# Kernel optimization log

Hardware: AMD Instinct MI355X
Metric: run time of the kernel (lower is better)

## Reference

```python
import jax, jax.numpy as jnp
import numpy as np

# Model dims (match init_kwargs / input_specs)
T, N, E, F_IN, F_OUT, BW = 16, 50000, 131072, 64, 64, 3


def setup_inputs() -> dict:
    key = jax.random.key(0)
    ks = jax.random.split(key, 6)
    x = jax.random.normal(ks[0], (T, N, F_IN), dtype=jnp.float32)
    M = jax.random.normal(ks[1], (T, T), dtype=jnp.float32)
    adj_rows = jax.random.randint(ks[2], (T, E), 0, N, dtype=jnp.int32)
    adj_cols = jax.random.randint(ks[3], (T, E), 0, N, dtype=jnp.int32)
    adj_vals = jax.random.uniform(ks[4], (T, E), dtype=jnp.float32)
    lim = float(np.sqrt(6.0 / (F_IN + F_OUT)))  # xavier_uniform
    weight = jax.random.uniform(ks[5], (F_IN, F_OUT), minval=-lim, maxval=lim, dtype=jnp.float32)
    return {"x": x, "M": M, "adj_vals": adj_vals, "weight": weight,
            "adj_rows": adj_rows, "adj_cols": adj_cols}


def _spmm(vals, rows, cols, x):
    # COO sparse [N,N] @ dense [N,F]: gather source rows, scatter-add to dest rows.
    return jax.ops.segment_sum(vals[:, None] * x[cols], rows, num_segments=x.shape[0])


def reference(x, M, adj_vals, weight, adj_rows, adj_cols):
    Tn, Nn, F = x.shape
    # Xt = M @ X (full M, as in compute_AtXt)
    Xt = (M @ x.reshape(Tn, -1)).reshape(Tn, Nn, F)
    k_idx = jnp.arange(Tn)
    AtXt = jnp.zeros((Tn, Nn, F), dtype=x.dtype)
    # Banded combination: At[k] = sum_{d=0}^{BW-1, k-d>=0} M[k, k-d] * A[k-d]
    # so At[k] @ Xt[k] = sum_d M[k,k-d] * (A[k-d] @ Xt[k])  -- avoids materializing At.
    for d in range(BW):
        j = k_idx - d
        valid = j >= 0
        jc = jnp.maximum(j, 0)
        w = jnp.where(valid, M[k_idx, jc], 0.0)  # [T] banded weights
        contrib = jax.vmap(_spmm)(adj_vals[jc], adj_rows[jc], adj_cols[jc], Xt)  # [T,N,F]
        AtXt = AtXt + w[:, None, None] * contrib
    # dropout is identity in eval mode; final dense projection
    return AtXt @ weight  # [T, N, F_OUT]
```

## Files before the change

kernel.cpp:

```cpp
#include <hip/hip_runtime.h>

#define TT 16
#define NN 50000
#define FF 64
#define EE 131072
#define NEDGE (TT*EE)
#define RPB 32
#define NRANGE ((NN + RPB - 1) / RPB)
#define NSUB 8
#define BCAP 256
#define NBUCK (NRANGE*NSUB)
#define SLOTS (NSUB*BCAP)
#define EMAX 1791
#define TAILI (EMAX*2)
#define K1BLKS 6250
#define APPBLKS (NEDGE/256)

typedef __attribute__((ext_vector_type(8))) short bf16x8;
typedef __attribute__((ext_vector_type(4))) short bf16x4;
typedef __attribute__((ext_vector_type(4))) float f32x4;
typedef __attribute__((ext_vector_type(2))) int   i32x2;
typedef __attribute__((ext_vector_type(2))) unsigned u32x2;

__device__ __forceinline__ unsigned pack2bf(float a, float b) {
    unsigned ua = __float_as_uint(a) + 0x8000u;
    unsigned ub = __float_as_uint(b) + 0x8000u;
    return __builtin_amdgcn_perm(ub, ua, 0x07060302u);
}
__device__ __forceinline__ float lo16f(unsigned u) { return __uint_as_float(u << 16); }
__device__ __forceinline__ float hi16f(unsigned u) { return __uint_as_float(u & 0xFFFF0000u); }

union U8 { unsigned u[4]; bf16x8 v; };
union U4 { unsigned u[2]; bf16x4 v; };

__device__ __forceinline__ f32x4 mfma16x16x16bf16(bf16x4 a, bf16x4 b, f32x4 c) {
#if __has_builtin(__builtin_amdgcn_mfma_f32_16x16x16bf16_1k)
    return __builtin_amdgcn_mfma_f32_16x16x16bf16_1k(a, b, c, 0, 0, 0);
#elif __has_builtin(__builtin_amdgcn_mfma_f32_16x16x16_bf16)
    return __builtin_amdgcn_mfma_f32_16x16x16_bf16(a, b, c, 0, 0, 0);
#else
    f32x4 d;
    asm volatile("v_mfma_f32_16x16x16_bf16 %0, %1, %2, %3\n\ts_nop 7\n\ts_nop 7"
                 : "=&v"(d) : "v"(a), "v"(b), "v"(c));
    return d;
#endif
}

__global__ __launch_bounds__(256) void k1_append(
    const float* __restrict__ x, const float* __restrict__ M,
    const float* __restrict__ W, unsigned short* __restrict__ Yt,
    const int* __restrict__ rows, const int* __restrict__ cols,
    const float* __restrict__ vals, int* __restrict__ bcnt,
    i32x2* __restrict__ btmp)
{
    if (blockIdx.x < K1BLKS) {
        const int tid  = threadIdx.x;
        const int wid  = tid >> 6;
        const int lane = tid & 63;
        const int col  = lane & 15;
        const int grp  = lane >> 4;

        bf16x8 bw[2][4];
#pragma unroll
        for (int q = 0; q < 2; ++q)
#pragma unroll
            for (int t = 0; t < 4; ++t) {
                U8 w8;
#pragma unroll
                for (int p = 0; p < 4; ++p)
                    w8.u[p] = pack2bf(W[(q*32 + grp*8 + 2*p)*FF + t*16 + col],
                                      W[(q*32 + grp*8 + 2*p + 1)*FF + t*16 + col]);
                bw[q][t] = w8.v;
            }

        U4 m4;
        m4.u[0] = pack2bf(M[col*16 + grp*4 + 0], M[col*16 + grp*4 + 1]);
        m4.u[1] = pack2bf(M[col*16 + grp*4 + 2], M[col*16 + grp*4 + 3]);
        const bf16x4 mf = m4.v;

        const f32x4 zero = {0.f, 0.f, 0.f, 0.f};
        const int node = (blockIdx.x*4 + wid)*2;
        const size_t lane_off = (size_t)col*NN*FF + grp*8;

        const float* xa = x + lane_off + (size_t)node*FF;
        f32x4 va0 = __builtin_nontemporal_load(reinterpret_cast<const f32x4*>(xa));
        f32x4 va1 = __builtin_nontemporal_load(reinterpret_cast<const f32x4*>(xa + 4));
        f32x4 va2 = __builtin_nontemporal_load(reinterpret_cast<const f32x4*>(xa + 32));
        f32x4 va3 = __builtin_nontemporal_load(reinterpret_cast<const f32x4*>(xa + 36));
        f32x4 vb0 = __builtin_nontemporal_load(reinterpret_cast<const f32x4*>(xa + 64));
        f32x4 vb1 = __builtin_nontemporal_load(reinterpret_cast<const f32x4*>(xa + 68));
        f32x4 vb2 = __builtin_nontemporal_load(reinterpret_cast<const f32x4*>(xa + 96));
        f32x4 vb3 = __builtin_nontemporal_load(reinterpret_cast<const f32x4*>(xa + 100));

#pragma unroll
        for (int n2 = 0; n2 < 2; ++n2) {
            U8 a0, a1;
            if (n2 == 0) {
                a0.u[0] = pack2bf(va0[0], va0[1]); a0.u[1] = pack2bf(va0[2], va0[3]);
                a0.u[2] = pack2bf(va1[0], va1[1]); a0.u[3] = pack2bf(va1[2], va1[3]);
                a1.u[0] = pack2bf(va2[0], va2[1]); a1.u[1] = pack2bf(va2[2], va2[3]);
                a1.u[2] = pack2bf(va3[0], va3[1]); a1.u[3] = pack2bf(va3[2], va3[3]);
            } else {
                a0.u[0] = pack2bf(vb0[0], vb0[1]); a0.u[1] = pack2bf(vb0[2], vb0[3]);
                a0.u[2] = pack2bf(vb1[0], vb1[1]); a0.u[3] = pack2bf(vb1[2], vb1[3]);
                a1.u[0] = pack2bf(vb2[0], vb2[1]); a1.u[1] = pack2bf(vb2[2], vb2[3]);
                a1.u[2] = pack2bf(vb3[0], vb3[1]); a1.u[3] = pack2bf(vb3[2], vb3[3]);
            }
            f32x4 acc[4];
#pragma unroll
            for (int t = 0; t < 4; ++t) acc[t] = zero;
#pragma unroll
            for (int t = 0; t < 4; ++t)
                acc[t] = __builtin_amdgcn_mfma_f32_16x16x32_bf16(a0.v, bw[0][t], acc[t], 0, 0, 0);
#pragma unroll
            for (int t = 0; t < 4; ++t)
                acc[t] = __builtin_amdgcn_mfma_f32_16x16x32_bf16(a1.v, bw[1][t], acc[t], 0, 0, 0);
#pragma unroll
            for (int t = 0; t < 4; ++t) {
                U4 pb;
                pb.u[0] = pack2bf(acc[t][0], acc[t][1]);
                pb.u[1] = pack2bf(acc[t][2], acc[t][3]);
                f32x4 y = mfma16x16x16bf16(pb.v, mf, zero);
                u32x2 st;
                st[0] = pack2bf(y[0], y[1]);
                st[1] = pack2bf(y[2], y[3]);
                *reinterpret_cast<u32x2*>(Yt + (size_t)(node + n2)*1024 + col*64 + t*16 + grp*4) = st;
            }
        }
    } else {
        const int i = (blockIdx.x - K1BLKS)*256 + threadIdx.x;
        const int r = __builtin_nontemporal_load(rows + i);
        const int j = i >> 17;
        const int b = (r >> 5)*NSUB + (blockIdx.x & 7);
        const int pos = atomicAdd(&bcnt[b], 1);
        if (pos < BCAP) {
            i32x2 e;
            e[0] = __builtin_nontemporal_load(cols + i) | (((r & 31)*16 + j) << 16);
            e[1] = __float_as_int(__builtin_nontemporal_load(vals + i));
            btmp[(size_t)b*BCAP + pos] = e;
        }
    }
}

__global__ __launch_bounds__(256) void sort_kernel(
    const int* __restrict__ bcnt, i32x2* __restrict__ btmp)
{
    __shared__ i32x2 sbuf[SLOTS];
    __shared__ int scnt[512], soff[512], scur[512], pscan[256];

    const int tid = threadIdx.x;
    const int blk = blockIdx.x;
    i32x2* region = btmp + (size_t)blk*SLOTS;

    scnt[tid] = 0; scnt[tid + 256] = 0;
    __syncthreads();

    int bc[NSUB]; i32x2 ent[NSUB];
#pragma unroll
    for (int s = 0; s < NSUB; ++s) {
        int c = bcnt[blk*NSUB + s];
        bc[s] = c < BCAP ? c : BCAP;
    }
#pragma unroll
    for (int s = 0; s < NSUB; ++s)
        if (tid < bc[s]) {
            ent[s] = region[s*BCAP + tid];
            atomicAdd(&scnt[((unsigned)ent[s][0]) >> 16], 1);
        }
    __syncthreads();

    const int a0 = scnt[2*tid], a1 = scnt[2*tid + 1];
    const int ps = a0 + a1;
    pscan[tid] = ps;
    __syncthreads();
    for (int o = 1; o < 256; o <<= 1) {
        int v = (tid >= o) ? pscan[tid - o] : 0;
        __syncthreads();
        pscan[tid] += v;
        __syncthreads();
    }
    const int excl = pscan[tid] - ps;
    soff[2*tid] = excl;      soff[2*tid + 1] = excl + a0;
    scur[2*tid] = excl;      scur[2*tid + 1] = excl + a0;
    __syncthreads();

#pragma unroll
    for (int s = 0; s < NSUB; ++s)
        if (tid < bc[s]) {
            const int key = ((unsigned)ent[s][0]) >> 16;
            const int pos = atomicAdd(&scur[key], 1);
            i32x2 se; se[0] = ent[s][0] & 0xFFFF; se[1] = ent[s][1];
            sbuf[pos] = se;
        }
    __syncthreads();

    const int total = soff[511] + scnt[511];
    const int lim = total < EMAX ? total : EMAX;
    for (int i = tid; i < lim; i += 256) region[i] = sbuf[i];
    int* tail = (int*)region + TAILI;
    tail[tid] = soff[tid];
    tail[tid + 256] = soff[tid + 256];
    if (tid == 0) tail[512] = lim;
}

template<int J>
__device__ __forceinline__ void k2_batch(int p0, int nj, int sbase, int esub, int fq,
    const i32x2* eb, const unsigned short* __restrict__ Yt,
    const float* __restrict__ M, f32x4* acc)
{
    const int p = p0 + esub;
    const bool act = p < nj;
    const int li = act ? (sbase + p) : 0;
    const i32x2 ent = eb[li];
    const float v = act ? __int_as_float(ent[1]) : 0.f;
    const int node = act ? ent[0] : 0;
    const unsigned short* yb = Yt + (size_t)node*1024 + J*64 + fq*4;
    {
        const u32x2 uv = *reinterpret_cast<const u32x2*>(yb);
        const float wv = M[J*17] * v;
        acc[J][0] = fmaf(wv, lo16f(uv[0]), acc[J][0]);
        acc[J][1] = fmaf(wv, hi16f(uv[0]), acc[J][1]);
        acc[J][2] = fmaf(wv, lo16f(uv[1]), acc[J][2]);
        acc[J][3] = fmaf(wv, hi16f(uv[1]), acc[J][3]);
    }
    if constexpr (J < 15) {
        const u32x2 uv = *reinterpret_cast<const u32x2*>(yb + 64);
        const float wv = M[J*17 + 16] * v;
        acc[J+1][0] = fmaf(wv, lo16f(uv[0]), acc[J+1][0]);
        acc[J+1][1] = fmaf(wv, hi16f(uv[0]), acc[J+1][1]);
        acc[J+1][2] = fmaf(wv, lo16f(uv[1]), acc[J+1][2]);
        acc[J+1][3] = fmaf(wv, hi16f(uv[1]), acc[J+1][3]);
    }
    if constexpr (J < 14) {
        const u32x2 uv = *reinterpret_cast<const u32x2*>(yb + 128);
        const float wv = M[J*17 + 32] * v;
        acc[J+2][0] = fmaf(wv, lo16f(uv[0]), acc[J+2][0]);
        acc[J+2][1] = fmaf(wv, hi16f(uv[0]), acc[J+2][1]);
        acc[J+2][2] = fmaf(wv, lo16f(uv[1]), acc[J+2][2]);
        acc[J+2][3] = fmaf(wv, hi16f(uv[1]), acc[J+2][3]);
    }
}

__global__ __launch_bounds__(256) void k2_gather(
    const unsigned short* __restrict__ Yt, const float* __restrict__ M,
    const i32x2* __restrict__ btmp, float* __restrict__ out)
{
    __shared__ i32x2 ebuf[4][128];
    const int tid  = threadIdx.x;
    const int wid  = tid >> 6;
    const int lane = tid & 63;
    const int esub = lane >> 4;
    const int fq   = lane & 15;
    const int r   = blockIdx.x*4 + wid;
    const int blk = r >> 5;
    const int rl  = r & 31;

    const i32x2* region = btmp + (size_t)blk*SLOTS;
    const int* tail = (const int*)region + TAILI;
    int o_l = 0;
    if (lane < 17) o_l = tail[rl*16 + lane];
    int off[17];
#pragma unroll
    for (int j = 0; j < 17; ++j) off[j] = __builtin_amdgcn_readlane(o_l, j);
    int ntot = off[16] - off[0];
    ntot = ntot < 128 ? ntot : 128;
    const i32x2* rowsrc = region + off[0];

    i32x2* eb = ebuf[wid];
    if (lane < ntot)      eb[lane]      = rowsrc[lane];
    if (lane + 64 < ntot) eb[lane + 64] = rowsrc[lane + 64];

    int c[16], sb[16];
#pragma unroll
    for (int j = 0; j < 16; ++j) {
        c[j]  = off[j+1] - off[j];
        sb[j] = off[j] - off[0];
    }

    f32x4 acc[16];
#pragma unroll
    for (int k = 0; k < 16; ++k) acc[k] = (f32x4){0.f, 0.f, 0.f, 0.f};

#define P1(J) k2_batch<J>(0, c[J], sb[J], esub, fq, eb, Yt, M, acc);
    P1(0)  P1(1)  P1(2)  P1(3)  P1(4)  P1(5)  P1(6)  P1(7)
    P1(8)  P1(9)  P1(10) P1(11) P1(12) P1(13) P1(14) P1(15)
#undef P1
#define P2(J) for (int p0 = 4; p0 < c[J]; p0 += 4) \
        k2_batch<J>(p0, c[J], sb[J], esub, fq, eb, Yt, M, acc);
    P2(0)  P2(1)  P2(2)  P2(3)  P2(4)  P2(5)  P2(6)  P2(7)
    P2(8)  P2(9)  P2(10) P2(11) P2(12) P2(13) P2(14) P2(15)
#undef P2

#pragma unroll
    for (int k = 0; k < 16; ++k) {
#pragma unroll
        for (int u = 0; u < 4; ++u) {
            acc[k][u] += __shfl_xor(acc[k][u], 16);
            acc[k][u] += __shfl_xor(acc[k][u], 32);
        }
    }
    if (esub == 0) {
#pragma unroll
        for (int k = 0; k < 16; ++k) {
            *reinterpret_cast<f32x4*>(out + ((size_t)k*NN + r)*FF + fq*4) = acc[k];
        }
    }
}

extern "C" void kernel_launch(void* const* d_in, const int* in_sizes, int n_in,
                              void* d_out, int out_size, void* d_ws, size_t ws_size,
                              hipStream_t stream) {
    (void)in_sizes; (void)n_in; (void)out_size; (void)ws_size;
    const float* x     = (const float*)d_in[0];
    const float* M     = (const float*)d_in[1];
    const float* avals = (const float*)d_in[2];
    const float* W     = (const float*)d_in[3];
    const int*   arows = (const int*)d_in[4];
    const int*   acols = (const int*)d_in[5];
    float* out = (float*)d_out;

    char* ws = (char*)d_ws;
    size_t o = 0;
    unsigned short* Yt = (unsigned short*)(ws + o); o += (size_t)TT*NN*FF*2;
    o = (o + 255) & ~(size_t)255;
    int* bcnt = (int*)(ws + o); o += (size_t)NBUCK*4;  o = (o + 255) & ~(size_t)255;
    i32x2* btmp = (i32x2*)(ws + o);

    (void)hipMemsetAsync(bcnt, 0, (size_t)NBUCK*4, stream);
    hipLaunchKernelGGL(k1_append, dim3(K1BLKS + APPBLKS), dim3(256), 0, stream,
                       x, M, W, Yt, arows, acols, avals, bcnt, btmp);
    hipLaunchKernelGGL(sort_kernel, dim3(NRANGE), dim3(256), 0, stream, bcnt, btmp);
    hipLaunchKernelGGL(k2_gather, dim3(12500), dim3(256), 0, stream, Yt, M, btmp, out);
}
```

Baseline: 349.8 us.

## Split fused projection/append kernel into persistent projection and separate append kernels

Splits the combined kernel into two launches: a projection-plus-time-mix kernel and a separate edge-append kernel. The projection kernel becomes grid-stride over nodes with 2048 blocks, handling one node per wave iteration instead of two nodes per wave with all loads issued up front. Nontemporal loads are replaced with ordinary loads. This adds an extra launch and removes the overlap between the memory-bound projection and the atomic-heavy append, which may expose more serialized time.

```diff
diff --git a/kernel.cpp b/kernel.cpp
--- a/kernel.cpp
+++ b/kernel.cpp
@@ -13,7 +13,6 @@
 #define SLOTS (NSUB*BCAP)
 #define EMAX 1791
 #define TAILI (EMAX*2)
-#define K1BLKS 6250
 #define APPBLKS (NEDGE/256)
 
 typedef __attribute__((ext_vector_type(8))) short bf16x8;
@@ -46,99 +45,88 @@
 #endif
 }
 
-__global__ __launch_bounds__(256) void k1_append(
+__global__ __launch_bounds__(256) void k1_proj_mix(
     const float* __restrict__ x, const float* __restrict__ M,
-    const float* __restrict__ W, unsigned short* __restrict__ Yt,
+    const float* __restrict__ W, unsigned short* __restrict__ Yt)
+{
+    const int tid  = threadIdx.x;
+    const int wid  = tid >> 6;
+    const int lane = tid & 63;
+    const int col  = lane & 15;
+    const int grp  = lane >> 4;
+
+    bf16x8 bw[2][4];
+#pragma unroll
+    for (int q = 0; q < 2; ++q)
+#pragma unroll
+        for (int t = 0; t < 4; ++t) {
+            U8 w8;
+#pragma unroll
+            for (int p = 0; p < 4; ++p)
+                w8.u[p] = pack2bf(W[(q*32 + grp*8 + 2*p)*FF + t*16 + col],
+                                  W[(q*32 + grp*8 + 2*p + 1)*FF + t*16 + col]);
+            bw[q][t] = w8.v;
+        }
+
+    U4 m4;
+    m4.u[0] = pack2bf(M[col*16 + grp*4 + 0], M[col*16 + grp*4 + 1]);
+    m4.u[1] = pack2bf(M[col*16 + grp*4 + 2], M[col*16 + grp*4 + 3]);
+    const bf16x4 mf = m4.v;
+
+    const f32x4 zero = {0.f, 0.f, 0.f, 0.f};
+    const int nwaves = gridDim.x * 4;
+
+    for (int node = blockIdx.x*4 + wid; node < NN; node += nwaves) {
+        const float* xb = x + (size_t)col*NN*FF + (size_t)node*FF + grp*8;
+        float4 v0 = *reinterpret_cast<const float4*>(xb);
+        float4 v1 = *reinterpret_cast<const float4*>(xb + 4);
+        float4 v2 = *reinterpret_cast<const float4*>(xb + 32);
+        float4 v3 = *reinterpret_cast<const float4*>(xb + 36);
+        U8 a0, a1;
+        a0.u[0] = pack2bf(v0.x, v0.y); a0.u[1] = pack2bf(v0.z, v0.w);
+        a0.u[2] = pack2bf(v1.x, v1.y); a0.u[3] = pack2bf(v1.z, v1.w);
+        a1.u[0] = pack2bf(v2.x, v2.y); a1.u[1] = pack2bf(v2.z, v2.w);
+        a1.u[2] = pack2bf(v3.x, v3.y); a1.u[3] = pack2bf(v3.z, v3.w);
+
+        f32x4 acc[4];
+#pragma unroll
+        for (int t = 0; t < 4; ++t) acc[t] = zero;
+#pragma unroll
+        for (int t = 0; t < 4; ++t)
+            acc[t] = __builtin_amdgcn_mfma_f32_16x16x32_bf16(a0.v, bw[0][t], acc[t], 0, 0, 0);
+#pragma unroll
+        for (int t = 0; t < 4; ++t)
+            acc[t] = __builtin_amdgcn_mfma_f32_16x16x32_bf16(a1.v, bw[1][t], acc[t], 0, 0, 0);
+
+#pragma unroll
+        for (int t = 0; t < 4; ++t) {
+            U4 pb;
+            pb.u[0] = pack2bf(acc[t][0], acc[t][1]);
+            pb.u[1] = pack2bf(acc[t][2], acc[t][3]);
+            f32x4 y = mfma16x16x16bf16(pb.v, mf, zero);
+            u32x2 st;
+            st[0] = pack2bf(y[0], y[1]);
+            st[1] = pack2bf(y[2], y[3]);
+            *reinterpret_cast<u32x2*>(Yt + (size_t)node*1024 + col*64 + t*16 + grp*4) = st;
+        }
+    }
+}
+
+__global__ __launch_bounds__(256) void append_kernel(
     const int* __restrict__ rows, const int* __restrict__ cols,
     const float* __restrict__ vals, int* __restrict__ bcnt,
     i32x2* __restrict__ btmp)
 {
-    if (blockIdx.x < K1BLKS) {
-        const int tid  = threadIdx.x;
-        const int wid  = tid >> 6;
-        const int lane = tid & 63;
-        const int col  = lane & 15;
-        const int grp  = lane >> 4;
-
-        bf16x8 bw[2][4];
-#pragma unroll
-        for (int q = 0; q < 2; ++q)
-#pragma unroll
-            for (int t = 0; t < 4; ++t) {
-                U8 w8;
-#pragma unroll
-                for (int p = 0; p < 4; ++p)
-                    w8.u[p] = pack2bf(W[(q*32 + grp*8 + 2*p)*FF + t*16 + col],
-                                      W[(q*32 + grp*8 + 2*p + 1)*FF + t*16 + col]);
-                bw[q][t] = w8.v;
-            }
-
-        U4 m4;
-        m4.u[0] = pack2bf(M[col*16 + grp*4 + 0], M[col*16 + grp*4 + 1]);
-        m4.u[1] = pack2bf(M[col*16 + grp*4 + 2], M[col*16 + grp*4 + 3]);
-        const bf16x4 mf = m4.v;
-
-        const f32x4 zero = {0.f, 0.f, 0.f, 0.f};
-        const int node = (blockIdx.x*4 + wid)*2;
-        const size_t lane_off = (size_t)col*NN*FF + grp*8;
-
-        const float* xa = x + lane_off + (size_t)node*FF;
-        f32x4 va0 = __builtin_nontemporal_load(reinterpret_cast<const f32x4*>(xa));
-        f32x4 va1 = __builtin_nontemporal_load(reinterpret_cast<const f32x4*>(xa + 4));
-        f32x4 va2 = __builtin_nontemporal_load(reinterpret_cast<const f32x4*>(xa + 32));
-        f32x4 va3 = __builtin_nontemporal_load(reinterpret_cast<const f32x4*>(xa + 36));
-        f32x4 vb0 = __builtin_nontemporal_load(reinterpret_cast<const f32x4*>(xa + 64));
-        f32x4 vb1 = __builtin_nontemporal_load(reinterpret_cast<const f32x4*>(xa + 68));
-        f32x4 vb2 = __builtin_nontemporal_load(reinterpret_cast<const f32x4*>(xa + 96));
-        f32x4 vb3 = __builtin_nontemporal_load(reinterpret_cast<const f32x4*>(xa + 100));
-
-#pragma unroll
-        for (int n2 = 0; n2 < 2; ++n2) {
-            U8 a0, a1;
-            if (n2 == 0) {
-                a0.u[0] = pack2bf(va0[0], va0[1]); a0.u[1] = pack2bf(va0[2], va0[3]);
-                a0.u[2] = pack2bf(va1[0], va1[1]); a0.u[3] = pack2bf(va1[2], va1[3]);
-                a1.u[0] = pack2bf(va2[0], va2[1]); a1.u[1] = pack2bf(va2[2], va2[3]);
-                a1.u[2] = pack2bf(va3[0], va3[1]); a1.u[3] = pack2bf(va3[2], va3[3]);
-            } else {
-                a0.u[0] = pack2bf(vb0[0], vb0[1]); a0.u[1] = pack2bf(vb0[2], vb0[3]);
-                a0.u[2] = pack2bf(vb1[0], vb1[1]); a0.u[3] = pack2bf(vb1[2], vb1[3]);
-                a1.u[0] = pack2bf(vb2[0], vb2[1]); a1.u[1] = pack2bf(vb2[2], vb2[3]);
-                a1.u[2] = pack2bf(vb3[0], vb3[1]); a1.u[3] = pack2bf(vb3[2], vb3[3]);
-            }
-            f32x4 acc[4];
-#pragma unroll
-            for (int t = 0; t < 4; ++t) acc[t] = zero;
-#pragma unroll
-            for (int t = 0; t < 4; ++t)
-                acc[t] = __builtin_amdgcn_mfma_f32_16x16x32_bf16(a0.v, bw[0][t], acc[t], 0, 0, 0);
-#pragma unroll
-            for (int t = 0; t < 4; ++t)
-                acc[t] = __builtin_amdgcn_mfma_f32_16x16x32_bf16(a1.v, bw[1][t], acc[t], 0, 0, 0);
-#pragma unroll
-            for (int t = 0; t < 4; ++t) {
-                U4 pb;
-                pb.u[0] = pack2bf(acc[t][0], acc[t][1]);
-                pb.u[1] = pack2bf(acc[t][2], acc[t][3]);
-                f32x4 y = mfma16x16x16bf16(pb.v, mf, zero);
-                u32x2 st;
-                st[0] = pack2bf(y[0], y[1]);
-                st[1] = pack2bf(y[2], y[3]);
-                *reinterpret_cast<u32x2*>(Yt + (size_t)(node + n2)*1024 + col*64 + t*16 + grp*4) = st;
-            }
-        }
-    } else {
-        const int i = (blockIdx.x - K1BLKS)*256 + threadIdx.x;
-        const int r = __builtin_nontemporal_load(rows + i);
-        const int j = i >> 17;
-        const int b = (r >> 5)*NSUB + (blockIdx.x & 7);
-        const int pos = atomicAdd(&bcnt[b], 1);
-        if (pos < BCAP) {
-            i32x2 e;
-            e[0] = __builtin_nontemporal_load(cols + i) | (((r & 31)*16 + j) << 16);
-            e[1] = __float_as_int(__builtin_nontemporal_load(vals + i));
-            btmp[(size_t)b*BCAP + pos] = e;
-        }
+    const int i = blockIdx.x*256 + threadIdx.x;
+    const int r = rows[i];
+    const int j = i >> 17;
+    const int b = (r >> 5)*NSUB + (blockIdx.x & 7);
+    const int pos = atomicAdd(&bcnt[b], 1);
+    if (pos < BCAP) {
+        i32x2 e;
+        e[0] = cols[i] | (((r & 31)*16 + j) << 16);
+        e[1] = __float_as_int(vals[i]);
+        btmp[(size_t)b*BCAP + pos] = e;
     }
 }
 
@@ -327,8 +315,9 @@
     i32x2* btmp = (i32x2*)(ws + o);
 
     (void)hipMemsetAsync(bcnt, 0, (size_t)NBUCK*4, stream);
-    hipLaunchKernelGGL(k1_append, dim3(K1BLKS + APPBLKS), dim3(256), 0, stream,
-                       x, M, W, Yt, arows, acols, avals, bcnt, btmp);
+    hipLaunchKernelGGL(k1_proj_mix, dim3(2048), dim3(256), 0, stream, x, M, W, Yt);
+    hipLaunchKernelGGL(append_kernel, dim3(APPBLKS), dim3(256), 0, stream,
+                       arows, acols, avals, bcnt, btmp);
     hipLaunchKernelGGL(sort_kernel, dim3(NRANGE), dim3(256), 0, stream, bcnt, btmp);
     hipLaunchKernelGGL(k2_gather, dim3(12500), dim3(256), 0, stream, Yt, M, btmp, out);
 }
```

Measured after the change: 361.4 us. 1.03x slower.
